# Optimization experiments

Measured on AMD Instinct MI355X. Metric: run time of the kernel, lower is better.

## Reference

```python
import jax, jax.numpy as jnp
import numpy as np
import math

KMAX = 4
K_FLOOR = 1e-6
NUM_GRAPHS = 32

def _k_lattice():
    r = np.arange(-KMAX, KMAX + 1)
    I, J, Kk = np.meshgrid(r, r, r, indexing='ij')
    lat = np.stack([I, J, Kk], axis=-1).reshape(-1, 3).astype(np.float32)
    lat = lat[np.any(lat != 0, axis=1)]  # exclude k=0 (include_k0=False)
    return jnp.asarray(lat)  # [K,3], K=728

def setup_inputs() -> dict:
    key = jax.random.key(0)
    ks = jax.random.split(key, 10)
    N, B, C, H = 8192, NUM_GRAPHS, 4, 64
    pos = jax.random.uniform(ks[0], (N, 3), dtype=jnp.float32) * 10.0
    batch = jnp.sort(jax.random.randint(ks[1], (N,), 0, B)).astype(jnp.int32)
    cell = jnp.eye(3, dtype=jnp.float32)[None] * 12.0 + 0.2 * jax.random.normal(ks[2], (B, 3, 3), dtype=jnp.float32)
    source = 0.1 * jax.random.normal(ks[3], (N, C), dtype=jnp.float32)
    W1 = jax.random.normal(ks[4], (3, H), dtype=jnp.float32) * (1.0 / math.sqrt(3))
    b1 = jnp.zeros((H,), jnp.float32)
    W2 = jax.random.normal(ks[5], (H, H), dtype=jnp.float32) * (1.0 / math.sqrt(H))
    b2 = jnp.zeros((H,), jnp.float32)
    W3 = jax.random.normal(ks[6], (H, 1), dtype=jnp.float32) * (1.0 / math.sqrt(H))
    b3 = jnp.zeros((1,), jnp.float32)
    return {"pos": pos, "batch": batch, "cell": cell, "source": source,
            "W1": W1, "b1": b1, "W2": W2, "b2": b2, "W3": W3, "b3": b3}

def reference(pos, batch, cell, source, W1, b1, W2, b2, W3, b3):
    two_pi = 2.0 * math.pi
    klat = _k_lattice()                              # [K,3]
    B = cell.shape[0]
    inv_cells = jnp.linalg.inv(cell)                 # [B,3,3]
    # fractional coords and phases
    frac = jnp.einsum('ni,nij->nj', pos, inv_cells[batch])   # [N,3]
    phases = two_pi * (frac @ klat.T)                # [N,K]
    cosP = jnp.cos(phases)
    sinP = jnp.sin(phases)
    # structure factors via segment-sum over graphs
    w_cos = source[:, None, :] * cosP[:, :, None]    # [N,K,C]
    w_sin = source[:, None, :] * sinP[:, :, None]
    S_cos = jax.ops.segment_sum(w_cos, batch, num_segments=B)  # [B,K,C]
    S_sin = jax.ops.segment_sum(w_sin, batch, num_segments=B)
    # k-space radial filter
    k_cart = two_pi * jnp.einsum('kd,bdh->bkh', klat, inv_cells)  # [B,K,3]
    k_norms = jnp.linalg.norm(k_cart, axis=-1)       # [B,K]
    safe_k = jnp.maximum(k_norms, K_FLOOR)
    x0 = jnp.log1p(safe_k)
    feat = jnp.stack([x0, x0 * x0, 1.0 / safe_k], axis=-1)       # [B,K,3]
    h = jax.nn.silu(feat @ W1 + b1)
    h = jax.nn.silu(h @ W2 + b2)
    scale = jax.nn.softplus((h @ W3 + b3)[..., 0])   # [B,K]
    w = (4.0 * math.pi / (safe_k * safe_k)) * scale
    w = jnp.where(k_norms > K_FLOOR, w, 0.0)         # include_k0=False
    volumes = jnp.maximum(jnp.abs(jnp.linalg.det(cell)), K_FLOOR)  # [B]
    # per-atom potential
    t_cos = w[batch] * cosP                          # [N,K]
    t_sin = w[batch] * sinP
    potential = (jnp.einsum('nk,nkc->nc', t_cos, S_cos[batch]) +
                 jnp.einsum('nk,nkc->nc', t_sin, S_sin[batch])) / volumes[batch][:, None]
    atom_energy = 0.5 * jnp.sum(source * potential, axis=-1, keepdims=True)  # [N,1]
    return atom_energy
```

## Files before the change

kernel.cpp:

```cpp
#include <hip/hip_runtime.h>
#include <math.h>

#define N_ATOMS 8192
#define NGRAPH  32
#define KHALF   364
#define TWO_PI  6.28318530717958647692f
#define CH      384


__device__ __forceinline__ float silu_f(float x) {
    return x / (1.0f + __expf(-x));
}

__device__ __forceinline__ void screv(float rev, float* s, float* c) {
    float f = rev - floorf(rev);
    *s = __builtin_amdgcn_sinf(f);
    *c = __builtin_amdgcn_cosf(f);
}

__device__ __forceinline__ void inv3x3(const float* __restrict__ c, float* iv, float* detOut) {
    float a00 = c[0], a01 = c[1], a02 = c[2];
    float a10 = c[3], a11 = c[4], a12 = c[5];
    float a20 = c[6], a21 = c[7], a22 = c[8];
    float c00 = a11 * a22 - a12 * a21;
    float c01 = a12 * a20 - a10 * a22;
    float c02 = a10 * a21 - a11 * a20;
    float det = a00 * c00 + a01 * c01 + a02 * c02;
    float r = 1.0f / det;
    iv[0] = c00 * r; iv[1] = (a02 * a21 - a01 * a22) * r; iv[2] = (a01 * a12 - a02 * a11) * r;
    iv[3] = c01 * r; iv[4] = (a00 * a22 - a02 * a20) * r; iv[5] = (a02 * a10 - a00 * a12) * r;
    iv[6] = c02 * r; iv[7] = (a01 * a20 - a00 * a21) * r; iv[8] = (a00 * a11 - a01 * a10) * r;
    *detOut = det;
}

__device__ __forceinline__ int lb_fast(const int* __restrict__ batch, int v, int lane) {
    if (v <= 0) return 0;
    if (v >= NGRAPH) return N_ATOMS;
    int g0 = v * 256 - 64;
    int y0 = batch[g0 + lane * 2];
    int y1 = batch[g0 + lane * 2 + 1];
    int x  = batch[lane * 128];
    int cnt = __popcll(__ballot(y0 < v)) + __popcll(__ballot(y1 < v));
    if (cnt > 0 && cnt < 128) return g0 + cnt;
    int c1 = __popcll(__ballot(x < v));
    int lo = (c1 > 0 ? c1 - 1 : 0) * 128;
    int z0 = batch[lo + lane * 2];
    int z1 = batch[lo + lane * 2 + 1];
    return lo + __popcll(__ballot(z0 < v)) + __popcll(__ballot(z1 < v));
}

__device__ __forceinline__ void stage_atom(
    float2 (* __restrict__ atab)[17], float4* __restrict__ srcs, int a,
    float px, float py, float pz, float4 msrc, const float* __restrict__ iv,
    int g, int jA0, int jA1, int jB0, int jB1)
{
    float r1 = px * iv[0] + py * iv[3] + pz * iv[6];
    float r2 = px * iv[1] + py * iv[4] + pz * iv[7];
    float r3 = px * iv[2] + py * iv[5] + pz * iv[8];
    float s1, c1; screv(r1, &s1, &c1);
    float s2, c2; screv(r2, &s2, &c2);
    float s3, c3; screv(r3, &s3, &c3);
    float c1_2 = c1 * c1 - s1 * s1, s1_2 = 2.f * c1 * s1;
    float cg_, sg_;
    if (g == 1)      { cg_ = c1;   sg_ = s1; }
    else if (g == 2) { cg_ = c1_2; sg_ = s1_2; }
    else if (g == 3) { cg_ = c1_2 * c1 - s1_2 * s1; sg_ = s1_2 * c1 + c1_2 * s1; }
    else             { cg_ = c1_2 * c1_2 - s1_2 * s1_2; sg_ = 2.f * c1_2 * s1_2; }
    float fic = cg_, fis = -sg_;
    float c2_2 = c2 * c2 - s2 * s2, s2_2 = 2.f * c2 * s2;
    float c2_4 = c2_2 * c2_2 - s2_2 * s2_2, s2_4 = 2.f * c2_2 * s2_2;
    float bc, bs;
    if (jA0 == 0) { bc = c2_4; bs = -s2_4; } else { bc = c2; bs = s2; }
    float ec = fic * bc - fis * bs;
    float es = fic * bs + fis * bc;
    int slot = 1;
    for (int m = jA0; m < jA1; ++m) {
        atab[a][slot] = make_float2(ec, es); ++slot;
        float t = ec * c2 - es * s2; es = ec * s2 + es * c2; ec = t;
    }
    if (jB1 > jB0) {
        int q = 4 - jB0;
        float qc, qs;
        if (q == 4)      { qc = c2_4; qs = s2_4; }
        else if (q == 3) { qc = c2_2 * c2 - s2_2 * s2; qs = s2_2 * c2 + c2_2 * s2; }
        else if (q == 2) { qc = c2_2; qs = s2_2; }
        else             { qc = c2;   qs = s2; }
        ec = qc; es = -qs;
        for (int m = jB0; m < jB1; ++m) {
            atab[a][slot] = make_float2(ec, es); ++slot;
            float t = ec * c2 - es * s2; es = ec * s2 + es * c2; ec = t;
        }
    }
    float c3_2 = c3 * c3 - s3 * s3, s3_2 = 2.f * c3 * s3;
    float c3_4 = c3_2 * c3_2 - s3_2 * s3_2, s3_4 = 2.f * c3_2 * s3_2;
    ec = c3_4; es = -s3_4;
    #pragma unroll
    for (int m = 0; m < 9; ++m) {
        atab[a][7 + m] = make_float2(ec, es);
        float t = ec * c3 - es * s3; es = ec * s3 + es * c3; ec = t;
    }
    srcs[a] = msrc;
}

__global__ __launch_bounds__(512, 1) void kAll(
    const float* __restrict__ cell, const float* __restrict__ pos,
    const int* __restrict__ batch, const float* __restrict__ source,
    const float* __restrict__ W1, const float* __restrict__ b1,
    const float* __restrict__ W2, const float* __restrict__ b2,
    const float* __restrict__ W3, const float* __restrict__ b3,
    float* __restrict__ out)
{
    __shared__ float  lwts[4484];
    __shared__ float  h1s[4096];
    __shared__ float2 atab[CH][17];
    __shared__ float4 srcs[CH];
    __shared__ float4 partC[7][64];
    __shared__ float4 partS[7][64];
    __shared__ float  comb[512];
    __shared__ float  lw[64];
    __shared__ float4 lSc[64];
    __shared__ float4 lSs[64];
    __shared__ int    sbounds[2];

    int bid = blockIdx.x;
    int tid = threadIdx.x;
    int gb = bid & 31;
    int b  = bid >> 5;

    int pA, jA0, jA1, jB0, jB1, nsegA, nel;
    if (b < 4) { pA = b;     jA0 = 0; jA1 = 5; jB0 = 0; jB1 = 0; nsegA = 45; nel = 45; }
    else       { pA = b - 4; jA0 = 5; jA1 = 9;
                 jB0 = b - 4; jB1 = (b == 7) ? 5 : (b - 3);
                 nsegA = 36; nel = 36 + (jB1 - jB0) * 9; }
    int nrows = (jA1 - jA0) + (jB1 - jB0);
    int g = 4 - pA;

    int kl = tid & 63;
    int h  = tid >> 6;

    float wa = 0.f, wb = 0.f, wc = 0.f, wd = 0.f;
    if (h < 6) {
        int wbase = gb * 256 - 64;
        if (wbase < 0) wbase = 0;
        if (wbase > N_ATOMS - CH) wbase = N_ATOMS - CH;
        for (int i = tid; i < 672; i += 384) {
            float4 v;
            if (i < 288) v = ((const float4*)pos)[(wbase * 3) / 4 + i];
            else         v = ((const float4*)source)[wbase + i - 288];
            wa += v.x; wb += v.y; wc += v.z; wd += v.w;
        }
        for (int i = tid; i < 1120; i += 384) {
            float4 v; int o;
            if (i < 48)        { v = ((const float4*)W1)[i];      o = i * 4; }
            else if (i < 64)   { v = ((const float4*)b1)[i - 48]; o = 192 + (i - 48) * 4; }
            else if (i < 1088) { v = ((const float4*)W2)[i - 64]; o = 256 + (i - 64) * 4; }
            else if (i < 1104) { v = ((const float4*)b2)[i - 1088]; o = 4352 + (i - 1088) * 4; }
            else               { v = ((const float4*)W3)[i - 1104]; o = 4416 + (i - 1104) * 4; }
            *((float4*)&lwts[o]) = v;
        }
        if (tid == 0) lwts[4480] = b3[0];
        asm volatile("" :: "v"(wa), "v"(wb), "v"(wc), "v"(wd));
    } else {
        int lb = lb_fast(batch, gb + (h - 6), kl);
        if (kl == 0) sbounds[h - 6] = lb;
    }

    float iv[9]; float det;
    inv3x3(cell + gb * 9, iv, &det);
    float vol = fmaxf(fabsf(det), 1e-6f);

    int el = kl;
    int pe, jje, lle;
    if (el < nsegA) { pe = pA; jje = jA0 + el / 9; lle = el % 9; }
    else            { int e2 = el - nsegA; pe = 4; jje = jB0 + e2 / 9; lle = e2 % 9; }
    int rrl = el / 9;
    int hk = pe * 81 + jje * 9 + lle;
    bool evalid = (el < nel) && (hk < KHALF);

    __syncthreads();

    int s0 = sbounds[0], e0 = sbounds[1];
    int len = e0 - s0;
    int cnt0 = min(CH, len);
    bool multi = len > CH;

    float px0 = 0.f, py0 = 0.f, pz0 = 0.f;
    float4 msrc = make_float4(0.f, 0.f, 0.f, 0.f);
    if (tid < cnt0) {
        int n = s0 + tid;
        px0 = pos[n * 3]; py0 = pos[n * 3 + 1]; pz0 = pos[n * 3 + 2];
        msrc = ((const float4*)source)[n];
    }

    float kn, sk, f0, f1, f2;
    {
        float fi = (float)(pe - 4);
        float fj = (float)(jje - 4);
        float fl = (float)(lle - 4);
        float kx = TWO_PI * (fi * iv[0] + fj * iv[3] + fl * iv[6]);
        float ky = TWO_PI * (fi * iv[1] + fj * iv[4] + fl * iv[7]);
        float kz = TWO_PI * (fi * iv[2] + fj * iv[5] + fl * iv[8]);
        kn = sqrtf(kx * kx + ky * ky + kz * kz);
        sk = fmaxf(kn, 1e-6f);
        float x0 = log1pf(sk);
        f0 = x0; f1 = x0 * x0; f2 = 1.0f / sk;
    }

    {
        int i0 = h * 8;
        #pragma unroll
        for (int ii = 0; ii < 8; ++ii) {
            int i = i0 + ii;
            float a_ = lwts[192 + i] + f0 * lwts[i] + f1 * lwts[64 + i] + f2 * lwts[128 + i];
            h1s[i * 64 + kl] = silu_f(a_);
        }
    }
    __syncthreads();

    {
        float2 acc2[4];
        #pragma unroll
        for (int q = 0; q < 4; ++q)
            acc2[q] = *(const float2*)&lwts[4352 + h * 8 + q * 2];
        for (int i = 0; i < 64; ++i) {
            float hh = h1s[i * 64 + kl];
            const float2* w2 = (const float2*)&lwts[256 + i * 64 + h * 8];
            #pragma unroll
            for (int q = 0; q < 4; ++q) {
                float2 w = w2[q];
                acc2[q].x = fmaf(hh, w.x, acc2[q].x);
                acc2[q].y = fmaf(hh, w.y, acc2[q].y);
            }
        }
        float partial = 0.f;
        #pragma unroll
        for (int q = 0; q < 4; ++q) {
            partial += silu_f(acc2[q].x) * lwts[4416 + h * 8 + q * 2];
            partial += silu_f(acc2[q].y) * lwts[4416 + h * 8 + q * 2 + 1];
        }
        comb[tid] = partial;
    }

    if (tid < cnt0)
        stage_atom(atab, srcs, tid, px0, py0, pz0, msrc, iv, g, jA0, jA1, jB0, jB1);
    __syncthreads();

    float4 accC = make_float4(0.f, 0.f, 0.f, 0.f);
    float4 accS = make_float4(0.f, 0.f, 0.f, 0.f);
    if (evalid) {
        for (int a = h; a < cnt0; a += 8) {
            float2 rj = atab[a][1 + rrl];
            float2 tl = atab[a][7 + lle];
            float cv = rj.x * tl.x - rj.y * tl.y;
            float sv = rj.x * tl.y + rj.y * tl.x;
            float4 s = srcs[a];
            accC.x = fmaf(s.x, cv, accC.x); accC.y = fmaf(s.y, cv, accC.y);
            accC.z = fmaf(s.z, cv, accC.z); accC.w = fmaf(s.w, cv, accC.w);
            accS.x = fmaf(s.x, sv, accS.x); accS.y = fmaf(s.y, sv, accS.y);
            accS.z = fmaf(s.z, sv, accS.z); accS.w = fmaf(s.w, sv, accS.w);
        }
    }

    for (int base = s0 + CH; base < e0; base += CH) {
        int cnt = min(CH, e0 - base);
        __syncthreads();
        if (tid < cnt) {
            int n = base + tid;
            float px = pos[n * 3], py = pos[n * 3 + 1], pz = pos[n * 3 + 2];
            float4 ms = ((const float4*)source)[n];
            stage_atom(atab, srcs, tid, px, py, pz, ms, iv, g, jA0, jA1, jB0, jB1);
        }
        __syncthreads();
        if (evalid) {
            for (int a = h; a < cnt; a += 8) {
                float2 rj = atab[a][1 + rrl];
                float2 tl = atab[a][7 + lle];
                float cv = rj.x * tl.x - rj.y * tl.y;
                float sv = rj.x * tl.y + rj.y * tl.x;
                float4 s = srcs[a];
                accC.x = fmaf(s.x, cv, accC.x); accC.y = fmaf(s.y, cv, accC.y);
                accC.z = fmaf(s.z, cv, accC.z); accC.w = fmaf(s.w, cv, accC.w);
                accS.x = fmaf(s.x, sv, accS.x); accS.y = fmaf(s.y, sv, accS.y);
                accS.z = fmaf(s.z, sv, accS.z); accS.w = fmaf(s.w, sv, accS.w);
            }
        }
    }

    if (h > 0) {
        partC[h - 1][kl] = accC;
        partS[h - 1][kl] = accS;
    }
    __syncthreads();
    if (h == 0) {
        #pragma unroll
        for (int qq = 0; qq < 7; ++qq) {
            float4 pc = partC[qq][kl], ps = partS[qq][kl];
            accC.x += pc.x; accC.y += pc.y; accC.z += pc.z; accC.w += pc.w;
            accS.x += ps.x; accS.y += ps.y; accS.z += ps.z; accS.w += ps.w;
        }
        lSc[kl] = accC;
        lSs[kl] = accS;
    } else if (h == 1) {
        float mlp = lwts[4480];
        #pragma unroll
        for (int w = 0; w < 8; ++w) mlp += comb[kl + 64 * w];
        float sc = (mlp > 20.0f) ? mlp : log1pf(__expf(mlp));
        float wgt = (12.566370614359172954f / (sk * sk)) * sc;
        if (!(kn > 1e-6f)) wgt = 0.0f;
        lw[kl] = evalid ? (wgt / vol) : 0.0f;
    }
    __syncthreads();

    int half = tid >> 8;
    int rsplit = (nrows + 1) >> 1;
    int r0 = half ? rsplit : 0;
    int r1 = half ? nrows  : rsplit;

    if (!multi) {
        for (int na = (tid & 255); na < len; na += 256) {
            float4 s = srcs[na];
            float2 tlv[9];
            #pragma unroll
            for (int ll = 0; ll < 9; ++ll) tlv[ll] = atab[na][7 + ll];
            float acc = 0.f;
            for (int rr = r0; rr < r1; ++rr) {
                float2 rj = atab[na][1 + rr];
                #pragma unroll
                for (int ll = 0; ll < 9; ++ll) {
                    float2 tl = tlv[ll];
                    float fc = rj.x * tl.x - rj.y * tl.y;
                    float fs = rj.x * tl.y + rj.y * tl.x;
                    int e = rr * 9 + ll;
                    float4 C  = lSc[e];
                    float4 S4 = lSs[e];
                    float w_  = lw[e];
                    float dc = s.x * C.x  + s.y * C.y  + s.z * C.z  + s.w * C.w;
                    float ds = s.x * S4.x + s.y * S4.y + s.z * S4.z + s.w * S4.w;
                    acc = fmaf(w_, fmaf(fc, dc, fs * ds), acc);
                }
            }
            atomicAdd(&out[s0 + na], acc);
        }
    } else {
        for (int na = (tid & 255); na < len; na += 256) {
            int n = s0 + na;
            float px = pos[n * 3], py = pos[n * 3 + 1], pz = pos[n * 3 + 2];
            float r1v = px * iv[0] + py * iv[3] + pz * iv[6];
            float r2v = px * iv[1] + py * iv[4] + pz * iv[7];
            float r3v = px * iv[2] + py * iv[5] + pz * iv[8];
            float s1, c1; screv(r1v, &s1, &c1);
            float s2, c2; screv(r2v, &s2, &c2);
            float s3, c3; screv(r3v, &s3, &c3);
            float c3_2 = c3 * c3 - s3 * s3, s3_2 = 2.f * c3 * s3;
            float c3_4 = c3_2 * c3_2 - s3_2 * s3_2, s3_4 = 2.f * c3_2 * s3_2;
            float c2_2 = c2 * c2 - s2 * s2, s2_2 = 2.f * c2 * s2;
            float c2_4 = c2_2 * c2_2 - s2_2 * s2_2, s2_4 = 2.f * c2_2 * s2_2;
            float4 s = ((const float4*)source)[n];
            float acc = 0.f;
            int rr = 0;
            {
                float c1_2 = c1 * c1 - s1 * s1, s1_2 = 2.f * c1 * s1;
                float cg_, sg_;
                if (g == 1)      { cg_ = c1;   sg_ = s1; }
                else if (g == 2) { cg_ = c1_2; sg_ = s1_2; }
                else if (g == 3) { cg_ = c1_2 * c1 - s1_2 * s1; sg_ = s1_2 * c1 + c1_2 * s1; }
                else             { cg_ = c1_2 * c1_2 - s1_2 * s1_2; sg_ = 2.f * c1_2 * s1_2; }
                float ci0 = cg_, si0 = -sg_;
                float ejc, ejs;
                if (jA0 == 0) { ejc = ci0 * c2_4 + si0 * s2_4; ejs = si0 * c2_4 - ci0 * s2_4; }
                else          { ejc = ci0 * c2 - si0 * s2;     ejs = si0 * c2 + ci0 * s2; }
                for (int jj = jA0; jj < jA1; ++jj, ++rr) {
                    if (rr >= r0 && rr < r1) {
                        float fc = ejc * c3_4 + ejs * s3_4;
                        float fs = ejs * c3_4 - ejc * s3_4;
                        #pragma unroll
                        for (int ll = 0; ll < 9; ++ll) {
                            int e = rr * 9 + ll;
                            float4 C  = lSc[e];
                            float4 S4 = lSs[e];
                            float w_  = lw[e];
                            float dc = s.x * C.x  + s.y * C.y  + s.z * C.z  + s.w * C.w;
                            float ds = s.x * S4.x + s.y * S4.y + s.z * S4.z + s.w * S4.w;
                            acc = fmaf(w_, fmaf(fc, dc, fs * ds), acc);
                            float nfc = fc * c3 - fs * s3;
                            fs = fc * s3 + fs * c3;
                            fc = nfc;
                        }
                    }
                    float t = ejc * c2 - ejs * s2; ejs = ejc * s2 + ejs * c2; ejc = t;
                }
            }
            if (jB1 > jB0) {
                float ejc = c2_4, ejs = -s2_4;
                for (int t2 = 0; t2 < jB0; ++t2) {
                    float t = ejc * c2 - ejs * s2; ejs = ejc * s2 + ejs * c2; ejc = t;
                }
                for (int jj = jB0; jj < jB1; ++jj, ++rr) {
                    if (rr >= r0 && rr < r1) {
                        float fc = ejc * c3_4 + ejs * s3_4;
                        float fs = ejs * c3_4 - ejc * s3_4;
                        #pragma unroll
                        for (int ll = 0; ll < 9; ++ll) {
                            int e = rr * 9 + ll;
                            float4 C  = lSc[e];
                            float4 S4 = lSs[e];
                            float w_  = lw[e];
                            float dc = s.x * C.x  + s.y * C.y  + s.z * C.z  + s.w * C.w;
                            float ds = s.x * S4.x + s.y * S4.y + s.z * S4.z + s.w * S4.w;
                            acc = fmaf(w_, fmaf(fc, dc, fs * ds), acc);
                            float nfc = fc * c3 - fs * s3;
                            fs = fc * s3 + fs * c3;
                            fc = nfc;
                        }
                    }
                    float t = ejc * c2 - ejs * s2; ejs = ejc * s2 + ejs * c2; ejc = t;
                }
            }
            atomicAdd(&out[n], acc);
        }
    }
}

extern "C" void kernel_launch(void* const* d_in, const int* in_sizes, int n_in,
                              void* d_out, int out_size, void* d_ws, size_t ws_size,
                              hipStream_t stream)
{
    const float* pos    = (const float*)d_in[0];
    const int*   batch  = (const int*)d_in[1];
    const float* cell   = (const float*)d_in[2];
    const float* source = (const float*)d_in[3];
    const float* W1 = (const float*)d_in[4];
    const float* b1 = (const float*)d_in[5];
    const float* W2 = (const float*)d_in[6];
    const float* b2 = (const float*)d_in[7];
    const float* W3 = (const float*)d_in[8];
    const float* b3 = (const float*)d_in[9];
    float* out = (float*)d_out;
    (void)d_ws; (void)ws_size;

    kAll<<<dim3(NGRAPH * 8), 512, 0, stream>>>(cell, pos, batch, source,
        W1, b1, W2, b2, W3, b3, out);
}
```

Before: 86.44 us.

## Double block size to 1024 threads and redistribute work across 16 wavegroups

Raises the block from 512 to 1024 threads and rebalances every phase for that size. The MLP hidden units are split 4 per group instead of 8, and the structure-factor atom loop strides by 16 instead of 8 with 15 partial buffers. The potential phase interleaves rows across 4 quarter-groups instead of 2 halves. The aim is more parallelism per graph block, since only 256 blocks run. The cost is higher register pressure under the new launch bound, more reduction work and shared memory, and dropping the per-thread cache of the 9 tl values in favour of LDS reloads.

```diff
diff --git a/kernel.cpp b/kernel.cpp
--- a/kernel.cpp
+++ b/kernel.cpp
@@ -102,7 +102,7 @@
     srcs[a] = msrc;
 }
 
-__global__ __launch_bounds__(512, 1) void kAll(
+__global__ __launch_bounds__(1024, 1) void kAll(
     const float* __restrict__ cell, const float* __restrict__ pos,
     const int* __restrict__ batch, const float* __restrict__ source,
     const float* __restrict__ W1, const float* __restrict__ b1,
@@ -114,9 +114,9 @@
     __shared__ float  h1s[4096];
     __shared__ float2 atab[CH][17];
     __shared__ float4 srcs[CH];
-    __shared__ float4 partC[7][64];
-    __shared__ float4 partS[7][64];
-    __shared__ float  comb[512];
+    __shared__ float4 partC[15][64];
+    __shared__ float4 partS[15][64];
+    __shared__ float  comb[1024];
     __shared__ float  lw[64];
     __shared__ float4 lSc[64];
     __shared__ float4 lSs[64];
@@ -139,17 +139,17 @@
     int h  = tid >> 6;
 
     float wa = 0.f, wb = 0.f, wc = 0.f, wd = 0.f;
-    if (h < 6) {
+    if (h < 14) {
         int wbase = gb * 256 - 64;
         if (wbase < 0) wbase = 0;
         if (wbase > N_ATOMS - CH) wbase = N_ATOMS - CH;
-        for (int i = tid; i < 672; i += 384) {
+        if (tid < 672) {
             float4 v;
-            if (i < 288) v = ((const float4*)pos)[(wbase * 3) / 4 + i];
-            else         v = ((const float4*)source)[wbase + i - 288];
-            wa += v.x; wb += v.y; wc += v.z; wd += v.w;
-        }
-        for (int i = tid; i < 1120; i += 384) {
+            if (tid < 288) v = ((const float4*)pos)[(wbase * 3) / 4 + tid];
+            else           v = ((const float4*)source)[wbase + tid - 288];
+            wa = v.x; wb = v.y; wc = v.z; wd = v.w;
+        }
+        for (int i = tid; i < 1120; i += 896) {
             float4 v; int o;
             if (i < 48)        { v = ((const float4*)W1)[i];      o = i * 4; }
             else if (i < 64)   { v = ((const float4*)b1)[i - 48]; o = 192 + (i - 48) * 4; }
@@ -161,8 +161,8 @@
         if (tid == 0) lwts[4480] = b3[0];
         asm volatile("" :: "v"(wa), "v"(wb), "v"(wc), "v"(wd));
     } else {
-        int lb = lb_fast(batch, gb + (h - 6), kl);
-        if (kl == 0) sbounds[h - 6] = lb;
+        int lb = lb_fast(batch, gb + (h - 14), kl);
+        if (kl == 0) sbounds[h - 14] = lb;
     }
 
     float iv[9]; float det;
@@ -207,9 +207,9 @@
     }
 
     {
-        int i0 = h * 8;
+        int i0 = h * 4;
         #pragma unroll
-        for (int ii = 0; ii < 8; ++ii) {
+        for (int ii = 0; ii < 4; ++ii) {
             int i = i0 + ii;
             float a_ = lwts[192 + i] + f0 * lwts[i] + f1 * lwts[64 + i] + f2 * lwts[128 + i];
             h1s[i * 64 + kl] = silu_f(a_);
@@ -218,26 +218,18 @@
     __syncthreads();
 
     {
-        float2 acc2[4];
+        float acc[4];
         #pragma unroll
-        for (int q = 0; q < 4; ++q)
-            acc2[q] = *(const float2*)&lwts[4352 + h * 8 + q * 2];
+        for (int j = 0; j < 4; ++j) acc[j] = lwts[4352 + h * 4 + j];
         for (int i = 0; i < 64; ++i) {
             float hh = h1s[i * 64 + kl];
-            const float2* w2 = (const float2*)&lwts[256 + i * 64 + h * 8];
+            const float* w2row = &lwts[256 + i * 64 + h * 4];
             #pragma unroll
-            for (int q = 0; q < 4; ++q) {
-                float2 w = w2[q];
-                acc2[q].x = fmaf(hh, w.x, acc2[q].x);
-                acc2[q].y = fmaf(hh, w.y, acc2[q].y);
-            }
+            for (int j = 0; j < 4; ++j) acc[j] = fmaf(hh, w2row[j], acc[j]);
         }
         float partial = 0.f;
         #pragma unroll
-        for (int q = 0; q < 4; ++q) {
-            partial += silu_f(acc2[q].x) * lwts[4416 + h * 8 + q * 2];
-            partial += silu_f(acc2[q].y) * lwts[4416 + h * 8 + q * 2 + 1];
-        }
+        for (int j = 0; j < 4; ++j) partial += silu_f(acc[j]) * lwts[4416 + h * 4 + j];
         comb[tid] = partial;
     }
 
@@ -248,7 +240,7 @@
     float4 accC = make_float4(0.f, 0.f, 0.f, 0.f);
     float4 accS = make_float4(0.f, 0.f, 0.f, 0.f);
     if (evalid) {
-        for (int a = h; a < cnt0; a += 8) {
+        for (int a = h; a < cnt0; a += 16) {
             float2 rj = atab[a][1 + rrl];
             float2 tl = atab[a][7 + lle];
             float cv = rj.x * tl.x - rj.y * tl.y;
@@ -272,7 +264,7 @@
         }
         __syncthreads();
         if (evalid) {
-            for (int a = h; a < cnt; a += 8) {
+            for (int a = h; a < cnt; a += 16) {
                 float2 rj = atab[a][1 + rrl];
                 float2 tl = atab[a][7 + lle];
                 float cv = rj.x * tl.x - rj.y * tl.y;
@@ -293,7 +285,7 @@
     __syncthreads();
     if (h == 0) {
         #pragma unroll
-        for (int qq = 0; qq < 7; ++qq) {
+        for (int qq = 0; qq < 15; ++qq) {
             float4 pc = partC[qq][kl], ps = partS[qq][kl];
             accC.x += pc.x; accC.y += pc.y; accC.z += pc.z; accC.w += pc.w;
             accS.x += ps.x; accS.y += ps.y; accS.z += ps.z; accS.w += ps.w;
@@ -303,7 +295,7 @@
     } else if (h == 1) {
         float mlp = lwts[4480];
         #pragma unroll
-        for (int w = 0; w < 8; ++w) mlp += comb[kl + 64 * w];
+        for (int w = 0; w < 16; ++w) mlp += comb[kl + 64 * w];
         float sc = (mlp > 20.0f) ? mlp : log1pf(__expf(mlp));
         float wgt = (12.566370614359172954f / (sk * sk)) * sc;
         if (!(kn > 1e-6f)) wgt = 0.0f;
@@ -311,23 +303,17 @@
     }
     __syncthreads();
 
-    int half = tid >> 8;
-    int rsplit = (nrows + 1) >> 1;
-    int r0 = half ? rsplit : 0;
-    int r1 = half ? nrows  : rsplit;
+    int q = tid >> 8;
 
     if (!multi) {
         for (int na = (tid & 255); na < len; na += 256) {
             float4 s = srcs[na];
-            float2 tlv[9];
-            #pragma unroll
-            for (int ll = 0; ll < 9; ++ll) tlv[ll] = atab[na][7 + ll];
             float acc = 0.f;
-            for (int rr = r0; rr < r1; ++rr) {
+            for (int rr = q; rr < nrows; rr += 4) {
                 float2 rj = atab[na][1 + rr];
                 #pragma unroll
                 for (int ll = 0; ll < 9; ++ll) {
-                    float2 tl = tlv[ll];
+                    float2 tl = atab[na][7 + ll];
                     float fc = rj.x * tl.x - rj.y * tl.y;
                     float fs = rj.x * tl.y + rj.y * tl.x;
                     int e = rr * 9 + ll;
@@ -370,7 +356,7 @@
                 if (jA0 == 0) { ejc = ci0 * c2_4 + si0 * s2_4; ejs = si0 * c2_4 - ci0 * s2_4; }
                 else          { ejc = ci0 * c2 - si0 * s2;     ejs = si0 * c2 + ci0 * s2; }
                 for (int jj = jA0; jj < jA1; ++jj, ++rr) {
-                    if (rr >= r0 && rr < r1) {
+                    if ((rr & 3) == q) {
                         float fc = ejc * c3_4 + ejs * s3_4;
                         float fs = ejs * c3_4 - ejc * s3_4;
                         #pragma unroll
@@ -396,7 +382,7 @@
                     float t = ejc * c2 - ejs * s2; ejs = ejc * s2 + ejs * c2; ejc = t;
                 }
                 for (int jj = jB0; jj < jB1; ++jj, ++rr) {
-                    if (rr >= r0 && rr < r1) {
+                    if ((rr & 3) == q) {
                         float fc = ejc * c3_4 + ejs * s3_4;
                         float fs = ejs * c3_4 - ejc * s3_4;
                         #pragma unroll
@@ -438,6 +424,6 @@
     float* out = (float*)d_out;
     (void)d_ws; (void)ws_size;
 
-    kAll<<<dim3(NGRAPH * 8), 512, 0, stream>>>(cell, pos, batch, source,
+    kAll<<<dim3(NGRAPH * 8), 1024, 0, stream>>>(cell, pos, batch, source,
         W1, b1, W2, b2, W3, b3, out);
 }
```

Result: no change. 86.11 us (-0.4%).
